# Kernel tuning notes

Hardware: AMD Instinct MI355X
Metric: run time of the kernel (lower is better)

Reference implementation:

```python
import jax, jax.numpy as jnp
import numpy as np

N = 100000   # nodes
E = 1600000  # edges
D = 128      # input feature dim
H = 128      # hidden dim
C = 10       # output classes
G = 64       # graphs in batch


def setup_inputs() -> dict:
    key = jax.random.key(0)
    ks = jax.random.split(key, 24)
    s = 0.02
    lin = lambda k, i, o: jax.random.normal(k, (i, o), jnp.float32) * s
    inp = {
        'x': jax.random.normal(ks[0], (N, D), jnp.float32),
        'edge_index': jax.random.randint(ks[1], (2, E), 0, N),
        'batch': jnp.sort(jax.random.randint(ks[2], (N,), 0, G)),
        # GIN conv 0: Linear(D,H)-ReLU-Linear(H,H)
        'w1_0': lin(ks[3], D, H), 'b1_0': jnp.zeros((H,), jnp.float32),
        'w2_0': lin(ks[4], H, H), 'b2_0': jnp.zeros((H,), jnp.float32),
        # GIN conv 1
        'w1_1': lin(ks[5], H, H), 'b1_1': jnp.zeros((H,), jnp.float32),
        'w2_1': lin(ks[6], H, H), 'b2_1': jnp.zeros((H,), jnp.float32),
        # GIN conv 2
        'w1_2': lin(ks[7], H, H), 'b1_2': jnp.zeros((H,), jnp.float32),
        'w2_2': lin(ks[8], H, H), 'b2_2': jnp.zeros((H,), jnp.float32),
        # LayerNorms (applied after layers 0 and 1)
        'ln_g0': jnp.ones((H,), jnp.float32), 'ln_b0': jnp.zeros((H,), jnp.float32),
        'ln_g1': jnp.ones((H,), jnp.float32), 'ln_b1': jnp.zeros((H,), jnp.float32),
        # post_mp: Linear(H,H) -> Dropout -> Linear(H,C)
        'pw1': lin(ks[9], H, H), 'pb1': jnp.zeros((H,), jnp.float32),
        'pw2': lin(ks[10], H, C), 'pb2': jnp.zeros((C,), jnp.float32),
    }
    return inp


def _gin_conv(x, src, dst, w1, b1, w2, b2):
    # GINConv with eps=0: MLP(x + sum_{j->i} x_j)
    agg = jax.ops.segment_sum(x[src], dst, num_segments=N)  # [N, d]
    h = x + agg
    h = jax.nn.relu(h @ w1 + b1) @ w2 + b2
    return h


def _layernorm(x, g, b, eps=1e-5):
    mu = jnp.mean(x, axis=-1, keepdims=True)
    var = jnp.var(x, axis=-1, keepdims=True)
    return (x - mu) * jax.lax.rsqrt(var + eps) * g + b


def reference(x, edge_index, batch,
              w1_0, b1_0, w2_0, b2_0,
              w1_1, b1_1, w2_1, b2_1,
              w1_2, b1_2, w2_2, b2_2,
              ln_g0, ln_b0, ln_g1, ln_b1,
              pw1, pb1, pw2, pb2):
    src, dst = edge_index[0], edge_index[1]
    convs = [(w1_0, b1_0, w2_0, b2_0), (w1_1, b1_1, w2_1, b2_1), (w1_2, b1_2, w2_2, b2_2)]
    lns = [(ln_g0, ln_b0), (ln_g1, ln_b1)]
    emb = x
    h = x
    for i in range(3):
        w1, b1, w2, b2 = convs[i]
        h = _gin_conv(h, src, dst, w1, b1, w2, b2)
        emb = h
        h = jax.nn.relu(h)
        # dropout p=0.25: identity in eval mode
        if i != 2:
            g, b = lns[i]
            h = _layernorm(h, g, b)
    # global mean pool over graphs
    sums = jax.ops.segment_sum(h, batch, num_segments=G)          # [G, H]
    cnts = jax.ops.segment_sum(jnp.ones((N,), h.dtype), batch, num_segments=G)
    pooled = sums / jnp.maximum(cnts, 1.0)[:, None]
    # post_mp (dropout identity in eval)
    z = pooled @ pw1 + pb1
    logits = z @ pw2 + pb2
    return emb, jax.nn.log_softmax(logits, axis=1)
```

## Files before the change

### kernel.cpp

```cpp
#include <hip/hip_runtime.h>

typedef __bf16 bf16_t;
typedef __bf16 bf16x8 __attribute__((ext_vector_type(8)));
typedef float floatx4 __attribute__((ext_vector_type(4)));

constexpr int N = 100000;
constexpr int E = 1600000;
constexpr int H = 128;
constexpr int G = 64;
constexpr int C = 10;
constexpr int NBLK = (N + 255) / 256;

constexpr int FPART = 8;
constexpr int FPART_SZ = (N + FPART - 1) / FPART;
constexpr int BCHUNK = 2048;
constexpr int BBLK = (E + BCHUNK - 1) / BCHUNK;
constexpr int BCAP = 204800;

__device__ inline float bflo(unsigned u) {
  return __builtin_bit_cast(float, u << 16);
}
__device__ inline float bfhi(unsigned u) {
  return __builtin_bit_cast(float, u & 0xffff0000u);
}
__device__ inline unsigned short f2b(float f) {
  return __builtin_bit_cast(unsigned short, (bf16_t)f);
}
__device__ inline unsigned pack2(float a, float b) {
  return (unsigned)f2b(a) | ((unsigned)f2b(b) << 16);
}

__global__ __launch_bounds__(256) void tobf_kernel(const float* __restrict__ x,
                                                   uint4* __restrict__ xb) {
  const int g = blockIdx.x * 256 + threadIdx.x;
  const float4 a = *(const float4*)(x + (size_t)g * 8);
  const float4 b = *(const float4*)(x + (size_t)g * 8 + 4);
  uint4 o;
  o.x = pack2(a.x, a.y);
  o.y = pack2(a.z, a.w);
  o.z = pack2(b.x, b.y);
  o.w = pack2(b.z, b.w);
  xb[g] = o;
}

__global__ __launch_bounds__(256) void bucket_kernel(
    const int* __restrict__ src, const int* __restrict__ dst,
    unsigned* __restrict__ buckets, int* __restrict__ bcnt) {
  __shared__ int offS[4][FPART];
  __shared__ int waveExcl[4][FPART];
  __shared__ int cntA[FPART];
  __shared__ int blockExcl[FPART];
  __shared__ int baseS[FPART];
  __shared__ unsigned stage[BCHUNK];
  const int tid = threadIdx.x;
  const int wave = tid >> 6;
  const int lane = tid & 63;
  if (tid < 32) ((int*)offS)[tid] = 0;
  __syncthreads();

  const int e0 = blockIdx.x * BCHUNK + tid * 8;
  int d[8], s[8];
  int nv = 0;
  if (e0 + 8 <= E) {
    const int4 da = *(const int4*)(dst + e0);
    const int4 db = *(const int4*)(dst + e0 + 4);
    const int4 sa = *(const int4*)(src + e0);
    const int4 sb = *(const int4*)(src + e0 + 4);
    d[0] = da.x; d[1] = da.y; d[2] = da.z; d[3] = da.w;
    d[4] = db.x; d[5] = db.y; d[6] = db.z; d[7] = db.w;
    s[0] = sa.x; s[1] = sa.y; s[2] = sa.z; s[3] = sa.w;
    s[4] = sb.x; s[5] = sb.y; s[6] = sb.z; s[7] = sb.w;
    nv = 8;
  } else {
    nv = (e0 < E) ? (E - e0) : 0;
    if (nv > 8) nv = 8;
    for (int j = 0; j < nv; ++j) {
      d[j] = dst[e0 + j];
      s[j] = src[e0 + j];
    }
    for (int j = nv; j < 8; ++j) { d[j] = 0; s[j] = 0; }
  }

  const unsigned long long below = (1ull << lane) - 1ull;

  int pj[8];
  int slotW[8];

#pragma unroll
  for (int j = 0; j < 8; ++j) {
    const bool valid = (j < nv);
    const int p = d[j] / FPART_SZ;
    pj[j] = p;
    unsigned long long mown = 0;
#pragma unroll
    for (int q = 0; q < FPART; ++q) {
      const unsigned long long mq = __ballot(valid && (p == q));
      if (p == q) mown = mq;
    }
    const int cnt = (int)__popcll(mown);
    const int rank = (int)__popcll(mown & below);
    const int base = offS[wave][p];
    if (valid && rank == 0) offS[wave][p] = base + cnt;
    slotW[j] = base + rank;
  }
  __syncthreads();

  if (tid < FPART) {
    int running = 0;
#pragma unroll
    for (int w = 0; w < 4; ++w) {
      waveExcl[w][tid] = running;
      running += offS[w][tid];
    }
    cntA[tid] = running;
    baseS[tid] = atomicAdd(&bcnt[tid], running);
  }
  __syncthreads();
  if (tid < FPART) {
    int ex = 0;
    for (int q = 0; q < tid; ++q) ex += cntA[q];
    blockExcl[tid] = ex;
  }
  __syncthreads();

#pragma unroll
  for (int j = 0; j < 8; ++j) {
    if (j < nv) {
      const int p = pj[j];
      stage[blockExcl[p] + waveExcl[wave][p] + slotW[j]] =
          ((unsigned)s[j] << 14) | (unsigned)(d[j] - p * FPART_SZ);
    }
  }
  __syncthreads();

#pragma unroll
  for (int p = 0; p < FPART; ++p) {
    const int c = cntA[p];
    const int gb = p * BCAP + baseS[p];
    const int lb = blockExcl[p];
    for (int i = tid; i < c; i += 256) buckets[gb + i] = stage[lb + i];
  }
}

__global__ __launch_bounds__(256) void deghist_kernel(
    const unsigned* __restrict__ buckets, const int* __restrict__ bcnt,
    int* __restrict__ deg) {
  __shared__ int cntS[FPART_SZ];
  const int part = blockIdx.x & (FPART - 1);
  const int sub = blockIdx.x >> 3;
  for (int i = threadIdx.x; i < FPART_SZ; i += 256) cntS[i] = 0;
  __syncthreads();
  const int cnt = bcnt[part];
  const int per = (cnt + 7) >> 3;
  const int lo = sub * per;
  const int hi = min(lo + per, cnt);
  const unsigned* b = buckets + part * BCAP;
  for (int i = lo + threadIdx.x; i < hi; i += 256)
    atomicAdd(&cntS[b[i] & 0x3FFFu], 1);
  __syncthreads();
  const int dbase = part * FPART_SZ;
  for (int i = threadIdx.x; i < FPART_SZ; i += 256) {
    const int c = cntS[i];
    if (c) atomicAdd(&deg[dbase + i], c);
  }
}

__global__ __launch_bounds__(256) void partial_kernel(
    const int* __restrict__ deg, int* __restrict__ partials) {
  __shared__ int sm[256];
  const int tid = threadIdx.x;
  const int i = blockIdx.x * 256 + tid;
  sm[tid] = (i < N) ? deg[i] : 0;
  __syncthreads();
  for (int off = 128; off > 0; off >>= 1) {
    if (tid < off) sm[tid] += sm[tid + off];
    __syncthreads();
  }
  if (tid == 0) partials[blockIdx.x] = sm[0];
}

__global__ __launch_bounds__(512) void scanp_kernel(
    const int* __restrict__ partials, int* __restrict__ blockbase) {
  __shared__ int p[512];
  const int t = threadIdx.x;
  p[t] = (t < NBLK) ? partials[t] : 0;
  __syncthreads();
  for (int off = 1; off < 512; off <<= 1) {
    int v = 0;
    if (t >= off) v = p[t - off];
    __syncthreads();
    p[t] += v;
    __syncthreads();
  }
  if (t < NBLK) blockbase[t] = (t == 0) ? 0 : p[t - 1];
}

__global__ __launch_bounds__(256) void expand_kernel(
    const int* __restrict__ deg, const int* __restrict__ blockbase,
    int* __restrict__ rowptr, int* __restrict__ cursor) {
  __shared__ int sm[256];
  const int tid = threadIdx.x;
  const int i = blockIdx.x * 256 + tid;
  const int d = (i < N) ? deg[i] : 0;
  sm[tid] = d;
  __syncthreads();
  for (int off = 1; off < 256; off <<= 1) {
    int v = 0;
    if (tid >= off) v = sm[tid - off];
    __syncthreads();
    sm[tid] += v;
    __syncthreads();
  }
  const int excl = sm[tid] - d + blockbase[blockIdx.x];
  if (i < N) {
    rowptr[i] = excl;
    cursor[i] = excl;
  }
  if (i == N - 1) rowptr[N] = excl + d;
}

__global__ __launch_bounds__(256) void fill2_kernel(
    const unsigned* __restrict__ buckets, const int* __restrict__ bcnt,
    int* __restrict__ cursor, int* __restrict__ csr_src) {
  const int part = blockIdx.x & (FPART - 1);
  const int blk = blockIdx.x >> 3;
  const int nblk = gridDim.x >> 3;
  const int cnt = bcnt[part];
  const unsigned* b = buckets + part * BCAP;
  const int dbase = part * FPART_SZ;
  for (int i = blk * 256 + threadIdx.x; i < cnt; i += nblk * 256) {
    const unsigned u = b[i];
    const int d = dbase + (int)(u & 0x3FFFu);
    const int s = (int)(u >> 14);
    const int slot = atomicAdd(&cursor[d], 1);
    csr_src[slot] = s;
  }
}

__global__ __launch_bounds__(256) void gather_kernel(
    const uint4* __restrict__ h, const int* __restrict__ rowptr,
    const int* __restrict__ csr_src, uint4* __restrict__ pre) {
  const int node = blockIdx.x * 16 + (threadIdx.x >> 4);
  const int l = threadIdx.x & 15;
  const int r0 = rowptr[node];
  const int r1 = rowptr[node + 1];
  const uint4 v = h[(size_t)node * 16 + l];
  float a0 = bflo(v.x), a1 = bfhi(v.x), a2 = bflo(v.y), a3 = bfhi(v.y);
  float a4 = bflo(v.z), a5 = bfhi(v.z), a6 = bflo(v.w), a7 = bfhi(v.w);
  int s = r0;
  for (; s + 3 < r1; s += 4) {
    const int i0 = csr_src[s], i1 = csr_src[s + 1];
    const int i2 = csr_src[s + 2], i3 = csr_src[s + 3];
    const uint4 u0 = h[(size_t)i0 * 16 + l];
    const uint4 u1 = h[(size_t)i1 * 16 + l];
    const uint4 u2 = h[(size_t)i2 * 16 + l];
    const uint4 u3 = h[(size_t)i3 * 16 + l];
    a0 += bflo(u0.x); a1 += bfhi(u0.x); a2 += bflo(u0.y); a3 += bfhi(u0.y);
    a4 += bflo(u0.z); a5 += bfhi(u0.z); a6 += bflo(u0.w); a7 += bfhi(u0.w);
    a0 += bflo(u1.x); a1 += bfhi(u1.x); a2 += bflo(u1.y); a3 += bfhi(u1.y);
    a4 += bflo(u1.z); a5 += bfhi(u1.z); a6 += bflo(u1.w); a7 += bfhi(u1.w);
    a0 += bflo(u2.x); a1 += bfhi(u2.x); a2 += bflo(u2.y); a3 += bfhi(u2.y);
    a4 += bflo(u2.z); a5 += bfhi(u2.z); a6 += bflo(u2.w); a7 += bfhi(u2.w);
    a0 += bflo(u3.x); a1 += bfhi(u3.x); a2 += bflo(u3.y); a3 += bfhi(u3.y);
    a4 += bflo(u3.z); a5 += bfhi(u3.z); a6 += bflo(u3.w); a7 += bfhi(u3.w);
  }
  for (; s < r1; ++s) {
    const uint4 u = h[(size_t)csr_src[s] * 16 + l];
    a0 += bflo(u.x); a1 += bfhi(u.x); a2 += bflo(u.y); a3 += bfhi(u.y);
    a4 += bflo(u.z); a5 += bfhi(u.z); a6 += bflo(u.w); a7 += bfhi(u.w);
  }
  uint4 o;
  o.x = pack2(a0, a1);
  o.y = pack2(a2, a3);
  o.z = pack2(a4, a5);
  o.w = pack2(a6, a7);
  pre[(size_t)node * 16 + l] = o;
}

template <int MODE>
__global__ __launch_bounds__(256) void mlp_kernel(
    const unsigned short* __restrict__ pre_g,
    const float* __restrict__ w1, const float* __restrict__ b1,
    const float* __restrict__ w2, const float* __restrict__ b2,
    const float* __restrict__ lng, const float* __restrict__ lnb,
    unsigned short* __restrict__ h_out,
    float* __restrict__ emb) {
  __shared__ unsigned short preS[32 * 136];
  __shared__ unsigned short hidS[32 * 136];
  __shared__ float muS[32];
  __shared__ float rsS[32];

  const int tid = threadIdx.x;
  const int wave = tid >> 6;
  const int lane = tid & 63;
  const int quad = lane >> 4;
  const int l16 = lane & 15;

  union F8 { bf16x8 v; bf16_t e[8]; };

  bf16x8 w1f[4][2], w2f[4][2];
#pragma unroll
  for (int nn = 0; nn < 2; ++nn) {
    const int col = wave * 32 + nn * 16 + l16;
#pragma unroll
    for (int kt = 0; kt < 4; ++kt) {
      F8 t1, t2;
#pragma unroll
      for (int j = 0; j < 8; ++j) {
        const int k = kt * 32 + quad * 8 + j;
        t1.e[j] = (bf16_t)w1[k * H + col];
        t2.e[j] = (bf16_t)w2[k * H + col];
      }
      w1f[kt][nn] = t1.v;
      w2f[kt][nn] = t2.v;
    }
  }
  const float b1v[2] = {b1[wave * 32 + l16], b1[wave * 32 + 16 + l16]};
  const float b2v[2] = {b2[wave * 32 + l16], b2[wave * 32 + 16 + l16]};
  float lng0 = 0.f, lng1 = 0.f, lnb0 = 0.f, lnb1 = 0.f;
  const int c2 = (tid * 2) & 127;
  if (MODE == 0) {
    lng0 = lng[c2]; lng1 = lng[c2 + 1];
    lnb0 = lnb[c2]; lnb1 = lnb[c2 + 1];
  }

  for (int tile = blockIdx.x; tile < N / 32; tile += gridDim.x) {
    const size_t base = (size_t)tile * 32 * H;
    {
      const uint4* srcp = (const uint4*)(pre_g + base);
#pragma unroll
      for (int it = 0; it < 2; ++it) {
        const int chunk = it * 256 + tid;
        const int row = chunk >> 4;
        const int colc = (chunk & 15) * 8;
        *(uint4*)&preS[row * 136 + colc] = srcp[chunk];
      }
    }
    __syncthreads();

    {
      floatx4 acc[2][2];
#pragma unroll
      for (int i = 0; i < 2; ++i)
#pragma unroll
        for (int j = 0; j < 2; ++j) acc[i][j] = {0.f, 0.f, 0.f, 0.f};
#pragma unroll
      for (int kt = 0; kt < 4; ++kt) {
        const int kc = kt * 32 + quad * 8;
        const bf16x8 a0 =
            __builtin_bit_cast(bf16x8, *(const uint4*)&preS[l16 * 136 + kc]);
        const bf16x8 a1 = __builtin_bit_cast(
            bf16x8, *(const uint4*)&preS[(16 + l16) * 136 + kc]);
        acc[0][0] = __builtin_amdgcn_mfma_f32_16x16x32_bf16(a0, w1f[kt][0],
                                                            acc[0][0], 0, 0, 0);
        acc[0][1] = __builtin_amdgcn_mfma_f32_16x16x32_bf16(a0, w1f[kt][1],
                                                            acc[0][1], 0, 0, 0);
        acc[1][0] = __builtin_amdgcn_mfma_f32_16x16x32_bf16(a1, w1f[kt][0],
                                                            acc[1][0], 0, 0, 0);
        acc[1][1] = __builtin_amdgcn_mfma_f32_16x16x32_bf16(a1, w1f[kt][1],
                                                            acc[1][1], 0, 0, 0);
      }
#pragma unroll
      for (int mt = 0; mt < 2; ++mt)
#pragma unroll
        for (int nn = 0; nn < 2; ++nn) {
          const int col = wave * 32 + nn * 16 + l16;
#pragma unroll
          for (int r = 0; r < 4; ++r) {
            const int row = mt * 16 + quad * 4 + r;
            const float v = fmaxf(acc[mt][nn][r] + b1v[nn], 0.f);
            hidS[row * 136 + col] = f2b(v);
          }
        }
    }
    __syncthreads();

    {
      floatx4 acc[2][2];
#pragma unroll
      for (int i = 0; i < 2; ++i)
#pragma unroll
        for (int j = 0; j < 2; ++j) acc[i][j] = {0.f, 0.f, 0.f, 0.f};
#pragma unroll
      for (int kt = 0; kt < 4; ++kt) {
        const int kc = kt * 32 + quad * 8;
        const bf16x8 a0 =
            __builtin_bit_cast(bf16x8, *(const uint4*)&hidS[l16 * 136 + kc]);
        const bf16x8 a1 = __builtin_bit_cast(
            bf16x8, *(const uint4*)&hidS[(16 + l16) * 136 + kc]);
        acc[0][0] = __builtin_amdgcn_mfma_f32_16x16x32_bf16(a0, w2f[kt][0],
                                                            acc[0][0], 0, 0, 0);
        acc[0][1] = __builtin_amdgcn_mfma_f32_16x16x32_bf16(a0, w2f[kt][1],
                                                            acc[0][1], 0, 0, 0);
        acc[1][0] = __builtin_amdgcn_mfma_f32_16x16x32_bf16(a1, w2f[kt][0],
                                                            acc[1][0], 0, 0, 0);
        acc[1][1] = __builtin_amdgcn_mfma_f32_16x16x32_bf16(a1, w2f[kt][1],
                                                            acc[1][1], 0, 0, 0);
      }
#pragma unroll
      for (int mt = 0; mt < 2; ++mt)
#pragma unroll
        for (int nn = 0; nn < 2; ++nn) {
          const int col = wave * 32 + nn * 16 + l16;
#pragma unroll
          for (int r = 0; r < 4; ++r) {
            const int row = mt * 16 + quad * 4 + r;
            float v = acc[mt][nn][r] + b2v[nn];
            if (MODE == 0) v = fmaxf(v, 0.f);
            preS[row * 136 + col] = f2b(v);
          }
        }
    }
    __syncthreads();

    if (MODE == 0) {
      const int n = tid >> 3;
      const int j = tid & 7;
      float s = 0.f, sq = 0.f;
#pragma unroll
      for (int t = 0; t < 16; ++t) {
        const float v =
            __builtin_bit_cast(float, (unsigned)preS[n * 136 + j + 8 * t] << 16);
        s += v;
        sq += v * v;
      }
      s += __shfl_xor(s, 1); sq += __shfl_xor(sq, 1);
      s += __shfl_xor(s, 2); sq += __shfl_xor(sq, 2);
      s += __shfl_xor(s, 4); sq += __shfl_xor(sq, 4);
      if (j == 0) {
        const float mu = s * (1.f / H);
        const float var = sq * (1.f / H) - mu * mu;
        muS[n] = mu;
        rsS[n] = rsqrtf(var + 1e-5f);
      }
      __syncthreads();
      unsigned* ho = (unsigned*)(h_out + base);
#pragma unroll
      for (int it = 0; it < 8; ++it) {
        const int idx = it * 512 + tid * 2;
        const int row = idx >> 7;
        const int k = idx & 127;
        const unsigned pr = *(const unsigned*)&preS[row * 136 + k];
        const float mu = muS[row], rs = rsS[row];
        const float v0 = (bflo(pr) - mu) * rs * lng0 + lnb0;
        const float v1 = (bfhi(pr) - mu) * rs * lng1 + lnb1;
        ho[idx >> 1] = pack2(v0, v1);
      }
    } else {
      unsigned* ho = (unsigned*)(h_out + base);
#pragma unroll
      for (int it = 0; it < 8; ++it) {
        const int idx = it * 512 + tid * 2;
        const int row = idx >> 7;
        const int k = idx & 127;
        const unsigned pr = *(const unsigned*)&preS[row * 136 + k];
        const float v0 = bflo(pr);
        const float v1 = bfhi(pr);
        *(float2*)&emb[base + idx] = make_float2(v0, v1);
        ho[idx >> 1] = pack2(fmaxf(v0, 0.f), fmaxf(v1, 0.f));
      }
    }
    __syncthreads();
  }
}

__global__ __launch_bounds__(256) void pool_kernel(
    const uint4* __restrict__ hv, const int* __restrict__ batch,
    float* __restrict__ pooled, float* __restrict__ cnt) {
  __shared__ int bs[256];
  __shared__ float smr[512];
  __shared__ int endS;
  const int tid = threadIdx.x;
  const int c0 = blockIdx.x * 256;
  const int len = min(256, N - c0);
  if (tid < len) bs[tid] = batch[c0 + tid];
  __syncthreads();

  const int nl = tid >> 4;
  const int fg = tid & 15;
  const int wave = tid >> 6;
  const int lane = tid & 63;

  int start = 0;
  while (start < len) {
    const int g = bs[start];
    if (tid == 0) endS = len;
    __syncthreads();
    for (int i = start + tid; i < len; i += 256)
      if (bs[i] != g) atomicMin(&endS, i);
    __syncthreads();
    const int end = endS;

    float a0 = 0.f, a1 = 0.f, a2 = 0.f, a3 = 0.f;
    float a4 = 0.f, a5 = 0.f, a6 = 0.f, a7 = 0.f;
    for (int i = start + nl; i < end; i += 16) {
      const uint4 u = hv[(size_t)(c0 + i) * 16 + fg];
      a0 += bflo(u.x); a1 += bfhi(u.x); a2 += bflo(u.y); a3 += bfhi(u.y);
      a4 += bflo(u.z); a5 += bfhi(u.z); a6 += bflo(u.w); a7 += bfhi(u.w);
    }
    a0 += __shfl_xor(a0, 16); a1 += __shfl_xor(a1, 16);
    a2 += __shfl_xor(a2, 16); a3 += __shfl_xor(a3, 16);
    a4 += __shfl_xor(a4, 16); a5 += __shfl_xor(a5, 16);
    a6 += __shfl_xor(a6, 16); a7 += __shfl_xor(a7, 16);
    a0 += __shfl_xor(a0, 32); a1 += __shfl_xor(a1, 32);
    a2 += __shfl_xor(a2, 32); a3 += __shfl_xor(a3, 32);
    a4 += __shfl_xor(a4, 32); a5 += __shfl_xor(a5, 32);
    a6 += __shfl_xor(a6, 32); a7 += __shfl_xor(a7, 32);
    if (lane < 16) {
      float* d = &smr[wave * 128 + lane * 8];
      d[0] = a0; d[1] = a1; d[2] = a2; d[3] = a3;
      d[4] = a4; d[5] = a5; d[6] = a6; d[7] = a7;
    }
    __syncthreads();
    if (tid < 128) {
      const float s =
          smr[tid] + smr[128 + tid] + smr[256 + tid] + smr[384 + tid];
      atomicAdd(&pooled[g * H + tid], s);
    }
    if (tid == 0) atomicAdd(&cnt[g], (float)(end - start));
    __syncthreads();
    start = end;
  }
}

__global__ __launch_bounds__(128) void head_kernel(
    const float* __restrict__ pooled, const float* __restrict__ cnt,
    const float* __restrict__ pw1, const float* __restrict__ pb1,
    const float* __restrict__ pw2, const float* __restrict__ pb2,
    float* __restrict__ out_logp) {
  __shared__ float p[H];
  __shared__ float z[H];
  __shared__ float l[C];
  const int g = blockIdx.x;
  const int f = threadIdx.x;
  const float c = fmaxf(cnt[g], 1.f);
  p[f] = pooled[g * H + f] / c;
  __syncthreads();
  float a = pb1[f];
  for (int k = 0; k < H; ++k) a += p[k] * pw1[k * H + f];
  z[f] = a;
  __syncthreads();
  if (f < C) {
    float a2 = pb2[f];
    for (int k = 0; k < H; ++k) a2 += z[k] * pw2[k * C + f];
    l[f] = a2;
  }
  __syncthreads();
  if (f == 0) {
    float m = l[0];
    for (int i = 1; i < C; ++i) m = fmaxf(m, l[i]);
    float s = 0.f;
    for (int i = 0; i < C; ++i) s += expf(l[i] - m);
    const float lse = m + logf(s);
    for (int i = 0; i < C; ++i) out_logp[g * C + i] = l[i] - lse;
  }
}

extern "C" void kernel_launch(void* const* d_in, const int* in_sizes, int n_in,
                              void* d_out, int out_size, void* d_ws,
                              size_t ws_size, hipStream_t stream) {
  const float* x = (const float*)d_in[0];
  const int* ei = (const int*)d_in[1];
  const int* src = ei;
  const int* dst = ei + E;
  const int* batch = (const int*)d_in[2];
  const float* w1_0 = (const float*)d_in[3];
  const float* b1_0 = (const float*)d_in[4];
  const float* w2_0 = (const float*)d_in[5];
  const float* b2_0 = (const float*)d_in[6];
  const float* w1_1 = (const float*)d_in[7];
  const float* b1_1 = (const float*)d_in[8];
  const float* w2_1 = (const float*)d_in[9];
  const float* b2_1 = (const float*)d_in[10];
  const float* w1_2 = (const float*)d_in[11];
  const float* b1_2 = (const float*)d_in[12];
  const float* w2_2 = (const float*)d_in[13];
  const float* b2_2 = (const float*)d_in[14];
  const float* ln_g0 = (const float*)d_in[15];
  const float* ln_b0 = (const float*)d_in[16];
  const float* ln_g1 = (const float*)d_in[17];
  const float* ln_b1 = (const float*)d_in[18];
  const float* pw1 = (const float*)d_in[19];
  const float* pb1 = (const float*)d_in[20];
  const float* pw2 = (const float*)d_in[21];
  const float* pb2 = (const float*)d_in[22];

  unsigned short* xb = (unsigned short*)d_ws;
  unsigned short* hb = xb + (size_t)N * H;
  unsigned short* pre = hb + (size_t)N * H;
  float* pooled = (float*)(pre + (size_t)N * H);
  float* cnt = pooled + (size_t)G * H;
  int* deg = (int*)(cnt + G);
  int* rowptr = deg + N;
  int* cursor = rowptr + N + 1;
  int* csr_src = cursor + N;
  int* partials = csr_src + E;
  int* blockbase = partials + NBLK;
  int* bcnt = blockbase + NBLK;
  unsigned* buckets = (unsigned*)pre;
  float* emb = (float*)d_out;
  float* logp = emb + (size_t)N * H;

  tobf_kernel<<<N * H / (256 * 8), 256, 0, stream>>>(x, (uint4*)xb);

  hipMemsetAsync(deg, 0, (size_t)N * sizeof(int), stream);
  hipMemsetAsync(bcnt, 0, (size_t)FPART * sizeof(int), stream);
  bucket_kernel<<<BBLK, 256, 0, stream>>>(src, dst, buckets, bcnt);
  deghist_kernel<<<64, 256, 0, stream>>>(buckets, bcnt, deg);
  partial_kernel<<<NBLK, 256, 0, stream>>>(deg, partials);
  scanp_kernel<<<1, 512, 0, stream>>>(partials, blockbase);
  expand_kernel<<<NBLK, 256, 0, stream>>>(deg, blockbase, rowptr, cursor);
  fill2_kernel<<<2048, 256, 0, stream>>>(buckets, bcnt, cursor, csr_src);

  gather_kernel<<<N / 16, 256, 0, stream>>>((const uint4*)xb, rowptr, csr_src,
                                            (uint4*)pre);
  mlp_kernel<0><<<2048, 256, 0, stream>>>(pre, w1_0, b1_0, w2_0, b2_0, ln_g0,
                                          ln_b0, hb, nullptr);
  gather_kernel<<<N / 16, 256, 0, stream>>>((const uint4*)hb, rowptr, csr_src,
                                            (uint4*)pre);
  mlp_kernel<0><<<2048, 256, 0, stream>>>(pre, w1_1, b1_1, w2_1, b2_1, ln_g1,
                                          ln_b1, hb, nullptr);
  gather_kernel<<<N / 16, 256, 0, stream>>>((const uint4*)hb, rowptr, csr_src,
                                            (uint4*)pre);
  mlp_kernel<1><<<2048, 256, 0, stream>>>(pre, w1_2, b1_2, w2_2, b2_2, nullptr,
                                          nullptr, hb, emb);

  hipMemsetAsync(pooled, 0, (size_t)(G * H + G) * sizeof(float), stream);
  pool_kernel<<<NBLK, 256, 0, stream>>>((const uint4*)hb, batch, pooled, cnt);
  head_kernel<<<G, 128, 0, stream>>>(pooled, cnt, pw1, pb1, pw2, pb2, logp);
}
```

Before: 551.4 us.

## Build CSR via two-level sub-bucketing with shared-memory local sort

Result: faster. 510.2 us (-7.5%).

```diff
diff --git a/kernel.cpp b/kernel.cpp
--- a/kernel.cpp
+++ b/kernel.cpp
@@ -16,6 +16,12 @@
 constexpr int BCHUNK = 2048;
 constexpr int BBLK = (E + BCHUNK - 1) / BCHUNK;
 constexpr int BCAP = 204800;
+
+constexpr int SUBP = 125;
+constexpr int SUBSZ = 100;
+constexpr int SB = FPART * SUBP;
+constexpr int SCAP = 2048;
+constexpr int SCHUNK = 8192;
 
 __device__ inline float bflo(unsigned u) {
   return __builtin_bit_cast(float, u << 16);
@@ -165,6 +171,65 @@
   }
 }
 
+__global__ __launch_bounds__(256) void subbucket_kernel(
+    const unsigned* __restrict__ buckets, const int* __restrict__ bcnt,
+    unsigned* __restrict__ subbuck, int* __restrict__ sbcnt) {
+  __shared__ unsigned stage[SCHUNK];
+  __shared__ int cntA[SUBP];
+  __shared__ int cntB[SUBP];
+  __shared__ int exclS[SUBP];
+  __shared__ int gbase[SUBP];
+  __shared__ int scanbuf[128];
+  const int part = blockIdx.x & (FPART - 1);
+  const int blk = blockIdx.x >> 3;
+  const int nblk = gridDim.x >> 3;
+  const int tid = threadIdx.x;
+  const int cnt = bcnt[part];
+  const unsigned* b = buckets + part * BCAP;
+
+  for (int c0 = blk * SCHUNK; c0 < cnt; c0 += nblk * SCHUNK) {
+    const int m = min(SCHUNK, cnt - c0);
+    if (tid < SUBP) {
+      cntA[tid] = 0;
+      cntB[tid] = 0;
+    }
+    __syncthreads();
+    for (int i = tid; i < m; i += 256) {
+      const unsigned ent = b[c0 + i];
+      atomicAdd(&cntA[(int)(ent & 0x3FFFu) / SUBSZ], 1);
+    }
+    __syncthreads();
+    if (tid < 128) scanbuf[tid] = (tid < SUBP) ? cntA[tid] : 0;
+    __syncthreads();
+    for (int off = 1; off < 128; off <<= 1) {
+      int v = 0;
+      if (tid < 128 && tid >= off) v = scanbuf[tid - off];
+      __syncthreads();
+      if (tid < 128) scanbuf[tid] += v;
+      __syncthreads();
+    }
+    if (tid < SUBP) {
+      exclS[tid] = scanbuf[tid] - cntA[tid];
+      gbase[tid] = atomicAdd(&sbcnt[part * SUBP + tid], cntA[tid]);
+    }
+    __syncthreads();
+    for (int i = tid; i < m; i += 256) {
+      const unsigned ent = b[c0 + i];
+      const int s = (int)(ent & 0x3FFFu) / SUBSZ;
+      const int r = atomicAdd(&cntB[s], 1);
+      stage[exclS[s] + r] = ent;
+    }
+    __syncthreads();
+    for (int i = tid; i < m; i += 256) {
+      const unsigned ent = stage[i];
+      const int s = (int)(ent & 0x3FFFu) / SUBSZ;
+      subbuck[(size_t)(part * SUBP + s) * SCAP + gbase[s] + (i - exclS[s])] =
+          ent;
+    }
+    __syncthreads();
+  }
+}
+
 __global__ __launch_bounds__(256) void partial_kernel(
     const int* __restrict__ deg, int* __restrict__ partials) {
   __shared__ int sm[256];
@@ -197,7 +262,7 @@
 
 __global__ __launch_bounds__(256) void expand_kernel(
     const int* __restrict__ deg, const int* __restrict__ blockbase,
-    int* __restrict__ rowptr, int* __restrict__ cursor) {
+    int* __restrict__ rowptr) {
   __shared__ int sm[256];
   const int tid = threadIdx.x;
   const int i = blockIdx.x * 256 + tid;
@@ -212,29 +277,57 @@
     __syncthreads();
   }
   const int excl = sm[tid] - d + blockbase[blockIdx.x];
-  if (i < N) {
-    rowptr[i] = excl;
-    cursor[i] = excl;
-  }
+  if (i < N) rowptr[i] = excl;
   if (i == N - 1) rowptr[N] = excl + d;
 }
 
-__global__ __launch_bounds__(256) void fill2_kernel(
-    const unsigned* __restrict__ buckets, const int* __restrict__ bcnt,
-    int* __restrict__ cursor, int* __restrict__ csr_src) {
-  const int part = blockIdx.x & (FPART - 1);
-  const int blk = blockIdx.x >> 3;
-  const int nblk = gridDim.x >> 3;
-  const int cnt = bcnt[part];
-  const unsigned* b = buckets + part * BCAP;
-  const int dbase = part * FPART_SZ;
-  for (int i = blk * 256 + threadIdx.x; i < cnt; i += nblk * 256) {
-    const unsigned u = b[i];
-    const int d = dbase + (int)(u & 0x3FFFu);
-    const int s = (int)(u >> 14);
-    const int slot = atomicAdd(&cursor[d], 1);
-    csr_src[slot] = s;
-  }
+__global__ __launch_bounds__(256) void fill3_kernel(
+    const unsigned* __restrict__ subbuck, const int* __restrict__ sbcnt,
+    const int* __restrict__ rowptr, int* __restrict__ csr_src) {
+  __shared__ unsigned ld[SCAP];
+  __shared__ int stageS[SCAP];
+  __shared__ int hist[SUBSZ];
+  __shared__ int cntB[SUBSZ];
+  __shared__ int exclS[SUBSZ];
+  __shared__ int scanbuf[128];
+  const int sb = blockIdx.x;
+  const int part = sb / SUBP;
+  const int subl = sb % SUBP;
+  const int n0 = part * FPART_SZ + subl * SUBSZ;
+  const int tid = threadIdx.x;
+  const int cnt = sbcnt[sb];
+  const unsigned* b = subbuck + (size_t)sb * SCAP;
+  if (tid < SUBSZ) {
+    hist[tid] = 0;
+    cntB[tid] = 0;
+  }
+  __syncthreads();
+  for (int i = tid; i < cnt; i += 256) {
+    const unsigned ent = b[i];
+    ld[i] = ent;
+    atomicAdd(&hist[(int)(ent & 0x3FFFu) - subl * SUBSZ], 1);
+  }
+  __syncthreads();
+  if (tid < 128) scanbuf[tid] = (tid < SUBSZ) ? hist[tid] : 0;
+  __syncthreads();
+  for (int off = 1; off < 128; off <<= 1) {
+    int v = 0;
+    if (tid < 128 && tid >= off) v = scanbuf[tid - off];
+    __syncthreads();
+    if (tid < 128) scanbuf[tid] += v;
+    __syncthreads();
+  }
+  if (tid < SUBSZ) exclS[tid] = scanbuf[tid] - hist[tid];
+  __syncthreads();
+  for (int i = tid; i < cnt; i += 256) {
+    const unsigned ent = ld[i];
+    const int j = (int)(ent & 0x3FFFu) - subl * SUBSZ;
+    const int r = atomicAdd(&cntB[j], 1);
+    stageS[exclS[j] + r] = (int)(ent >> 14);
+  }
+  __syncthreads();
+  const int rp0 = rowptr[n0];
+  for (int i = tid; i < cnt; i += 256) csr_src[rp0 + i] = stageS[i];
 }
 
 __global__ __launch_bounds__(256) void gather_kernel(
@@ -597,20 +690,23 @@
   int* partials = csr_src + E;
   int* blockbase = partials + NBLK;
   int* bcnt = blockbase + NBLK;
+  int* sbcnt = bcnt + FPART;
   unsigned* buckets = (unsigned*)pre;
+  unsigned* subbuck = buckets + (size_t)FPART * BCAP;
   float* emb = (float*)d_out;
   float* logp = emb + (size_t)N * H;
 
   tobf_kernel<<<N * H / (256 * 8), 256, 0, stream>>>(x, (uint4*)xb);
 
   hipMemsetAsync(deg, 0, (size_t)N * sizeof(int), stream);
-  hipMemsetAsync(bcnt, 0, (size_t)FPART * sizeof(int), stream);
+  hipMemsetAsync(bcnt, 0, (size_t)(FPART + SB) * sizeof(int), stream);
   bucket_kernel<<<BBLK, 256, 0, stream>>>(src, dst, buckets, bcnt);
   deghist_kernel<<<64, 256, 0, stream>>>(buckets, bcnt, deg);
+  subbucket_kernel<<<256, 256, 0, stream>>>(buckets, bcnt, subbuck, sbcnt);
   partial_kernel<<<NBLK, 256, 0, stream>>>(deg, partials);
   scanp_kernel<<<1, 512, 0, stream>>>(partials, blockbase);
-  expand_kernel<<<NBLK, 256, 0, stream>>>(deg, blockbase, rowptr, cursor);
-  fill2_kernel<<<2048, 256, 0, stream>>>(buckets, bcnt, cursor, csr_src);
+  expand_kernel<<<NBLK, 256, 0, stream>>>(deg, blockbase, rowptr);
+  fill3_kernel<<<SB, 256, 0, stream>>>(subbuck, sbcnt, rowptr, csr_src);
 
   gather_kernel<<<N / 16, 256, 0, stream>>>((const uint4*)xb, rowptr, csr_src,
                                             (uint4*)pre);
```
